# Performance work log

Hardware: AMD Instinct MI355X
Metric: run time of the kernel (lower is better)

Reference implementation:

```python
import jax, jax.numpy as jnp
import numpy as np

BETA = 0.1       # reputation weight
GAMMA = 0.1      # load penalty weight
EXPL_C = 0.1     # UCB exploration constant
LOAD_EMA = 0.9   # load EMA alpha
TOP_K = 2
EPS = 1e-10


def setup_inputs() -> dict:
    key = jax.random.key(0)
    k1, k2, k3, k4, k5 = jax.random.split(key, 5)
    B, S, H, E = 4, 4096, 2048, 64
    return {
        "x": jax.random.normal(k1, (B, S, H), dtype=jnp.float32),
        "gate_w": jax.random.normal(k2, (E, H), dtype=jnp.float32) * (1.0 / np.sqrt(H)),
        "reputation": jax.random.normal(k3, (E,), dtype=jnp.float32),
        "loads": jax.random.uniform(k4, (E,), dtype=jnp.float32),
        "counts": jax.random.uniform(k5, (E,), dtype=jnp.float32),
        "total_decisions": 1000000,
    }


def reference(x, gate_w, reputation, loads, counts, total_decisions):
    B, S, H = x.shape
    E = gate_w.shape[0]
    x_flat = x.reshape(-1, H)                                  # [T, H]
    base_logits = jnp.einsum("th,eh->te", x_flat, gate_w)      # [T, E]

    # current_batch_assignments is None -> current_loads = expert_loads
    updated_loads = LOAD_EMA * loads + (1.0 - LOAD_EMA) * loads  # [E]

    # UCB-style exploration bonus, broadcast over tokens
    expl = EXPL_C * jnp.sqrt(jnp.log(jnp.float32(total_decisions) + 1.0) / (counts + EPS))  # [E]

    selection_scores = (base_logits
                        + BETA * reputation[None, :]
                        - GAMMA * updated_loads[None, :]
                        + expl[None, :])                        # [T, E]

    top_k_scores, top_k_indices = jax.lax.top_k(selection_scores, TOP_K)  # [T, K]
    routing_weights = jax.nn.softmax(top_k_scores, axis=-1).reshape(B, S, TOP_K)
    expert_indices = top_k_indices.reshape(B, S, TOP_K)

    # differentiable load-balancing aux loss
    router_probs = jax.nn.softmax(selection_scores.astype(jnp.float32), axis=-1)  # [T, E]
    expert_gate = jax.nn.one_hot(top_k_indices, E, dtype=jnp.float32).sum(axis=1)  # [T, E]
    tokens_per_expert = expert_gate.mean(axis=0)               # [E]
    router_prob_per_expert = router_probs.mean(axis=0)         # [E]
    aux_loss = (tokens_per_expert * router_prob_per_expert).sum() * E

    return routing_weights, expert_indices, aux_loss
```

## Files before the change

kernel.cpp:

```cpp
#include <hip/hip_runtime.h>
#include <hip/hip_bf16.h>
#include <cmath>

#define HDIM 2048
#define H4   (HDIM / 4)
#define NEXP 64
#define TTOT 16384
#define BKC  64
#define NCHUNK (HDIM / BKC)
#define BTOK 32
#define NBLK (TTOT / BTOK)
#define LDT  72
#define LDS_SC 65

typedef unsigned short u16;
typedef short  bf16x8 __attribute__((ext_vector_type(8)));
typedef float  f32x16 __attribute__((ext_vector_type(16)));

#define WS_AUX_FLOATS  (2 * NBLK * NEXP)
#define WS_GWS_OFF     WS_AUX_FLOATS
#define GWS_FLOATS     (3 * NEXP * HDIM / 2)
#define WS_NEEDED_FLOATS (WS_GWS_OFF + GWS_FLOATS)
#define ESTR (NEXP * HDIM)

__device__ __forceinline__ unsigned cvtpk(float a, float b) {
    __hip_bfloat162 h2 = __float22bfloat162_rn(make_float2(a, b));
    unsigned r;
    __builtin_memcpy(&r, &h2, sizeof(r));
    return r;
}
__device__ __forceinline__ void split3(float4 f, uint2* H, uint2* M, uint2* L) {
    unsigned h0 = cvtpk(f.x, f.y), h1 = cvtpk(f.z, f.w);
    float r0 = f.x - __uint_as_float(h0 << 16);
    float r1 = f.y - __uint_as_float(h0 & 0xffff0000u);
    float r2 = f.z - __uint_as_float(h1 << 16);
    float r3 = f.w - __uint_as_float(h1 & 0xffff0000u);
    unsigned m0 = cvtpk(r0, r1), m1 = cvtpk(r2, r3);
    float s0 = r0 - __uint_as_float(m0 << 16);
    float s1 = r1 - __uint_as_float(m0 & 0xffff0000u);
    float s2 = r2 - __uint_as_float(m1 << 16);
    float s3 = r3 - __uint_as_float(m1 & 0xffff0000u);
    unsigned l0 = cvtpk(s0, s1), l1 = cvtpk(s2, s3);
    *H = make_uint2(h0, h1); *M = make_uint2(m0, m1); *L = make_uint2(l0, l1);
}

__global__ __launch_bounds__(256) void split_gw_k(
    const float* __restrict__ gw, u16* __restrict__ gws)
{
    const int i = blockIdx.x * 256 + threadIdx.x;
    float4 f = reinterpret_cast<const float4*>(gw)[i];
    uint2 h, m, l;
    split3(f, &h, &m, &l);
    reinterpret_cast<uint2*>(gws)[i]            = h;
    reinterpret_cast<uint2*>(gws + ESTR)[i]     = m;
    reinterpret_cast<uint2*>(gws + 2 * ESTR)[i] = l;
}

__global__ __launch_bounds__(256, 2) void router_fused2(
    const float* __restrict__ x,
    const u16*   __restrict__ gws,
    const float* __restrict__ rep,
    const float* __restrict__ loads,
    const float* __restrict__ counts,
    const int*   __restrict__ total_dec,
    float* __restrict__ out_w,
    float* __restrict__ out_idx,
    float* __restrict__ prob_part,
    float* __restrict__ gate_part)
{
    __shared__ __align__(16) char pool[(3 * BTOK * LDT + 3 * NEXP * LDT) * sizeof(short)];
    short (*aT)[BTOK][LDT] = reinterpret_cast<short (*)[BTOK][LDT]>(pool);
    short (*bT)[NEXP][LDT] =
        reinterpret_cast<short (*)[NEXP][LDT]>(pool + 3 * BTOK * LDT * sizeof(short));
    float (*sc_s)[LDS_SC] = reinterpret_cast<float (*)[LDS_SC]>(pool);
    __shared__ float bias_s[NEXP];
    __shared__ float m_s[BTOK], zi_s[BTOK];
    __shared__ int   i1_s[BTOK], i2_s[BTOK];

    const int tid  = threadIdx.x;
    const int lane = tid & 63;
    const int l31  = lane & 31;
    const int lhi  = lane >> 5;
    const int w    = tid >> 6;
    const int wn   = w & 1;
    const int kh   = w >> 1;
    const int rt   = blockIdx.x;
    const int T0   = rt * BTOK;

    if (tid < NEXP) {
        float L = logf((float)(*total_dec) + 1.0f);
        bias_s[tid] = 0.1f * rep[tid] - 0.1f * loads[tid]
                    + 0.1f * sqrtf(L / (counts[tid] + 1e-10f));
    }

    const int srow = tid >> 3;
    const int scol = tid & 7;
    const int grow = tid >> 2;
    const int gcol = tid & 3;

    const float4* __restrict__ x4 = reinterpret_cast<const float4*>(x)
        + (size_t)(T0 + srow) * H4 + scol * 2;
    const u16* __restrict__ gwsB = gws + (size_t)grow * HDIM + gcol * 16;

    f32x16 acc;
    #pragma unroll
    for (int i = 0; i < 16; ++i) acc[i] = 0.0f;

    const short* aP[3];
    const short* bP[3];
    #pragma unroll
    for (int v = 0; v < 3; ++v) {
        aP[v] = &aT[v][l31][8 * lhi];
        bP[v] = &bT[v][32 * wn + l31][8 * lhi];
    }

    float4 xa[2][2];

#define LOAD_CHUNK(CH, SLOT) do {                                              \
        xa[SLOT][0] = x4[(CH) * 16];                                           \
        xa[SLOT][1] = x4[(CH) * 16 + 1];                                       \
    } while (0)

    LOAD_CHUNK(0, 0);
    LOAD_CHUNK(1, 1);

    for (int ch = 0; ch < NCHUNK; ++ch) {
        const int slot = ch & 1;
        uint4 bq[3][2];
        #pragma unroll
        for (int v = 0; v < 3; ++v) {
            const u16* p = gwsB + (size_t)v * ESTR + ch * BKC;
            bq[v][0] = *reinterpret_cast<const uint4*>(p);
            bq[v][1] = *reinterpret_cast<const uint4*>(p + 8);
        }
        {
            uint2 h0, m0, l0, h1, m1, l1;
            split3(xa[slot][0], &h0, &m0, &l0);
            split3(xa[slot][1], &h1, &m1, &l1);
            const int kl = scol * 8;
            *reinterpret_cast<uint4*>(&aT[0][srow][kl]) =
                make_uint4(h0.x, h0.y, h1.x, h1.y);
            *reinterpret_cast<uint4*>(&aT[1][srow][kl]) =
                make_uint4(m0.x, m0.y, m1.x, m1.y);
            *reinterpret_cast<uint4*>(&aT[2][srow][kl]) =
                make_uint4(l0.x, l0.y, l1.x, l1.y);
        }
        if (ch + 2 < NCHUNK) LOAD_CHUNK(ch + 2, slot);
        #pragma unroll
        for (int v = 0; v < 3; ++v) {
            *reinterpret_cast<uint4*>(&bT[v][grow][gcol * 16])     = bq[v][0];
            *reinterpret_cast<uint4*>(&bT[v][grow][gcol * 16 + 8]) = bq[v][1];
        }
        __syncthreads();

        #pragma unroll
        for (int s = 0; s < 2; ++s) {
            const int ko = 16 * (2 * kh + s);
            bf16x8 ah = *reinterpret_cast<const bf16x8*>(aP[0] + ko);
            bf16x8 am = *reinterpret_cast<const bf16x8*>(aP[1] + ko);
            bf16x8 al = *reinterpret_cast<const bf16x8*>(aP[2] + ko);
            bf16x8 bh = *reinterpret_cast<const bf16x8*>(bP[0] + ko);
            bf16x8 bm = *reinterpret_cast<const bf16x8*>(bP[1] + ko);
            bf16x8 bl = *reinterpret_cast<const bf16x8*>(bP[2] + ko);
            acc = __builtin_amdgcn_mfma_f32_32x32x16_bf16(ah, bh, acc, 0, 0, 0);
            acc = __builtin_amdgcn_mfma_f32_32x32x16_bf16(ah, bm, acc, 0, 0, 0);
            acc = __builtin_amdgcn_mfma_f32_32x32x16_bf16(am, bh, acc, 0, 0, 0);
            acc = __builtin_amdgcn_mfma_f32_32x32x16_bf16(ah, bl, acc, 0, 0, 0);
            acc = __builtin_amdgcn_mfma_f32_32x32x16_bf16(am, bm, acc, 0, 0, 0);
            acc = __builtin_amdgcn_mfma_f32_32x32x16_bf16(al, bh, acc, 0, 0, 0);
        }
        __syncthreads();
    }
#undef LOAD_CHUNK

    const int e = 32 * wn + l31;
    if (kh == 0) {
        #pragma unroll
        for (int r = 0; r < 16; ++r) {
            const int t_loc = (r & 3) + 8 * (r >> 2) + 4 * lhi;
            sc_s[t_loc][e] = acc[r];
        }
    }
    __syncthreads();
    if (kh == 1) {
        #pragma unroll
        for (int r = 0; r < 16; ++r) {
            const int t_loc = (r & 3) + 8 * (r >> 2) + 4 * lhi;
            sc_s[t_loc][e] += acc[r] + bias_s[e];
        }
    }
    __syncthreads();

    if (tid < BTOK) {
        const int t = tid;
        float m1 = -INFINITY, m2 = -INFINITY;
        int   i1 = 0, i2 = 0;
        for (int ee = 0; ee < NEXP; ++ee) {
            const float s = sc_s[t][ee];
            if (s > m1)      { m2 = m1; i2 = i1; m1 = s; i1 = ee; }
            else if (s > m2) { m2 = s; i2 = ee; }
        }
        float z = 0.0f;
        for (int ee = 0; ee < NEXP; ++ee) z += __expf(sc_s[t][ee] - m1);

        const float e2  = expf(m2 - m1);
        const float inv = 1.0f / (1.0f + e2);
        const int   gt  = T0 + t;
        reinterpret_cast<float2*>(out_w)[gt]   = make_float2(inv, e2 * inv);
        reinterpret_cast<float2*>(out_idx)[gt] = make_float2((float)i1, (float)i2);
        m_s[t] = m1; zi_s[t] = 1.0f / z; i1_s[t] = i1; i2_s[t] = i2;
    }
    __syncthreads();

    if (tid < NEXP) {
        const int ee = tid;
        float ps = 0.0f, gs = 0.0f;
        for (int t = 0; t < BTOK; ++t) {
            ps += __expf(sc_s[t][ee] - m_s[t]) * zi_s[t];
            gs += (float)((i1_s[t] == ee) + (i2_s[t] == ee));
        }
        prob_part[rt * NEXP + ee] = ps;
        gate_part[rt * NEXP + ee] = gs;
    }
}

__global__ __launch_bounds__(256) void router_aux2(
    const float* __restrict__ prob_part,
    const float* __restrict__ gate_part,
    float* __restrict__ out_aux)
{
    __shared__ float rp[4][NEXP], rg[4][NEXP];
    const int e = threadIdx.x & 63;
    const int q = threadIdx.x >> 6;
    float sp = 0.0f, sg = 0.0f;
    for (int b = q * (NBLK / 4); b < (q + 1) * (NBLK / 4); ++b) {
        sp += prob_part[b * NEXP + e];
        sg += gate_part[b * NEXP + e];
    }
    rp[q][e] = sp; rg[q][e] = sg;
    __syncthreads();
    if (threadIdx.x < NEXP) {
        float pT = rp[0][e] + rp[1][e] + rp[2][e] + rp[3][e];
        float gT = rg[0][e] + rg[1][e] + rg[2][e] + rg[3][e];
        const float invT = 1.0f / (float)TTOT;
        float v = (gT * invT) * (pT * invT);
        #pragma unroll
        for (int off = 32; off > 0; off >>= 1)
            v += __shfl_down(v, off);
        if (e == 0) out_aux[0] = v * (float)NEXP;
    }
}

#define BKF  32
#define LDAF (64 + 4)
__global__ __launch_bounds__(256) void router_main(
    const float* __restrict__ x,
    const float* __restrict__ gw,
    const float* __restrict__ rep,
    const float* __restrict__ loads,
    const float* __restrict__ counts,
    const int*   __restrict__ total_dec,
    float* __restrict__ out_w,
    float* __restrict__ out_idx,
    float* __restrict__ prob_acc,
    float* __restrict__ gate_acc)
{
    __shared__ float a_s[2][BKF][LDAF];
    __shared__ float b_s[2][BKF][LDAF];
    __shared__ float sc_s[64][LDS_SC];
    __shared__ float bias_s[NEXP];
    __shared__ float m_s[64], z_s[64];
    __shared__ int   i1_s[64], i2_s[64];

    const int tid = threadIdx.x;
    const int tx  = tid & 15;
    const int ty  = tid >> 4;
    const int r0  = tid >> 3;
    const int c4  = tid & 7;
    const int t0  = blockIdx.x * 64;

    if (tid < NEXP) {
        float L = logf((float)(*total_dec) + 1.0f);
        bias_s[tid] = 0.1f * rep[tid] - 0.1f * loads[tid]
                    + 0.1f * sqrtf(L / (counts[tid] + 1e-10f));
    }

    const float4* __restrict__ x4 = reinterpret_cast<const float4*>(x) + (size_t)t0 * H4;
    const float4* __restrict__ g4 = reinterpret_cast<const float4*>(gw);

    float acc[4][4] = {};

#define STORE_TILE(BUFI, A0, A1, B0, B1) do {                                  \
        float _t0[4] = {(A0).x, (A0).y, (A0).z, (A0).w};                       \
        float _t1[4] = {(A1).x, (A1).y, (A1).z, (A1).w};                       \
        float _t2[4] = {(B0).x, (B0).y, (B0).z, (B0).w};                       \
        float _t3[4] = {(B1).x, (B1).y, (B1).z, (B1).w};                       \
        _Pragma("unroll")                                                      \
        for (int u = 0; u < 4; ++u) {                                          \
            a_s[BUFI][c4 * 4 + u][r0]      = _t0[u];                           \
            a_s[BUFI][c4 * 4 + u][r0 + 32] = _t1[u];                           \
            b_s[BUFI][c4 * 4 + u][r0]      = _t2[u];                           \
            b_s[BUFI][c4 * 4 + u][r0 + 32] = _t3[u];                           \
        } } while (0)

    {
        float4 a0 = x4[(size_t)r0 * H4 + c4];
        float4 a1 = x4[(size_t)(r0 + 32) * H4 + c4];
        float4 b0 = g4[(size_t)r0 * H4 + c4];
        float4 b1 = g4[(size_t)(r0 + 32) * H4 + c4];
        STORE_TILE(0, a0, a1, b0, b1);
    }
    __syncthreads();

    int buf = 0;
    for (int it = 0; it < HDIM / BKF; ++it) {
        float4 na0, na1, nb0, nb1;
        const bool has_next = (it + 1 < HDIM / BKF);
        if (has_next) {
            const int k4 = (it + 1) * (BKF / 4);
            na0 = x4[(size_t)r0 * H4 + k4 + c4];
            na1 = x4[(size_t)(r0 + 32) * H4 + k4 + c4];
            nb0 = g4[(size_t)r0 * H4 + k4 + c4];
            nb1 = g4[(size_t)(r0 + 32) * H4 + k4 + c4];
        }
        #pragma unroll
        for (int kk = 0; kk < BKF; ++kk) {
            const float4 afv = *reinterpret_cast<const float4*>(&a_s[buf][kk][ty * 4]);
            const float4 bfv = *reinterpret_cast<const float4*>(&b_s[buf][kk][tx * 4]);
            const float af[4] = {afv.x, afv.y, afv.z, afv.w};
            const float bf[4] = {bfv.x, bfv.y, bfv.z, bfv.w};
            #pragma unroll
            for (int i = 0; i < 4; ++i)
                #pragma unroll
                for (int j = 0; j < 4; ++j)
                    acc[i][j] = fmaf(af[i], bf[j], acc[i][j]);
        }
        if (has_next) STORE_TILE(buf ^ 1, na0, na1, nb0, nb1);
        __syncthreads();
        buf ^= 1;
    }
#undef STORE_TILE

    #pragma unroll
    for (int i = 0; i < 4; ++i)
        #pragma unroll
        for (int j = 0; j < 4; ++j)
            sc_s[ty * 4 + i][tx * 4 + j] = acc[i][j] + bias_s[tx * 4 + j];
    __syncthreads();

    if (tid < 64) {
        const int t = tid;
        float m1 = -INFINITY, m2 = -INFINITY;
        int   i1 = 0, i2 = 0;
        for (int e = 0; e < NEXP; ++e) {
            const float s = sc_s[t][e];
            if (s > m1)      { m2 = m1; i2 = i1; m1 = s; i1 = e; }
            else if (s > m2) { m2 = s; i2 = e; }
        }
        float z = 0.0f;
        for (int e = 0; e < NEXP; ++e) z += expf(sc_s[t][e] - m1);
        const float e2  = expf(m2 - m1);
        const float inv = 1.0f / (1.0f + e2);
        const int   gt  = t0 + t;
        reinterpret_cast<float2*>(out_w)[gt]   = make_float2(inv, e2 * inv);
        reinterpret_cast<float2*>(out_idx)[gt] = make_float2((float)i1, (float)i2);
        m_s[t] = m1; z_s[t] = z; i1_s[t] = i1; i2_s[t] = i2;
    }
    __syncthreads();

    if (tid < NEXP) {
        const int e = tid;
        float ps = 0.0f, gs = 0.0f;
        for (int t = 0; t < 64; ++t) {
            ps += expf(sc_s[t][e] - m_s[t]) / z_s[t];
            gs += (float)((i1_s[t] == e) + (i2_s[t] == e));
        }
        atomicAdd(&prob_acc[e], ps);
        atomicAdd(&gate_acc[e], gs);
    }
}

__global__ void router_aux(const float* __restrict__ prob_acc,
                           const float* __restrict__ gate_acc,
                           float* __restrict__ out_aux)
{
    const float invT = 1.0f / (float)TTOT;
    const int e = threadIdx.x;
    float v = (gate_acc[e] * invT) * (prob_acc[e] * invT);
    #pragma unroll
    for (int off = 32; off > 0; off >>= 1)
        v += __shfl_down(v, off);
    if (e == 0) out_aux[0] = v * (float)NEXP;
}

extern "C" void kernel_launch(void* const* d_in, const int* in_sizes, int n_in,
                              void* d_out, int out_size, void* d_ws, size_t ws_size,
                              hipStream_t stream)
{
    const float* x      = (const float*)d_in[0];
    const float* gw     = (const float*)d_in[1];
    const float* rep    = (const float*)d_in[2];
    const float* loads  = (const float*)d_in[3];
    const float* counts = (const float*)d_in[4];
    const int*   total  = (const int*)d_in[5];

    float* out     = (float*)d_out;
    float* out_w   = out;
    float* out_idx = out + 32768;
    float* out_aux = out + 65536;

    if (ws_size >= (size_t)WS_NEEDED_FLOATS * sizeof(float)) {
        float* prob_part = (float*)d_ws;
        float* gate_part = prob_part + NBLK * NEXP;
        u16*   gws       = (u16*)((float*)d_ws + WS_GWS_OFF);

        split_gw_k<<<dim3(NEXP * HDIM / 4 / 256), dim3(256), 0, stream>>>(gw, gws);
        router_fused2<<<dim3(NBLK), dim3(256), 0, stream>>>(
            x, gws, rep, loads, counts, total, out_w, out_idx, prob_part, gate_part);
        router_aux2<<<dim3(1), dim3(256), 0, stream>>>(prob_part, gate_part, out_aux);
    } else {
        float* prob_acc = (float*)d_ws;
        float* gate_acc = prob_acc + NEXP;
        (void)hipMemsetAsync(d_ws, 0, 2 * NEXP * sizeof(float), stream);
        router_main<<<dim3(TTOT / 64), dim3(256), 0, stream>>>(
            x, gw, rep, loads, counts, total, out_w, out_idx, prob_acc, gate_acc);
        router_aux<<<dim3(1), dim3(64), 0, stream>>>(prob_acc, gate_acc, out_aux);
    }
}
```

Before: 251.9 us.

## Double K-chunk size to 128 and prefetch next chunk's x and weights into registers

The K tile per iteration grows from 64 to 128 columns, which halves the number of barrier-separated iterations and doubles the MFMA work between syncs. The prefetch scheme also changes. Instead of a two-deep x register pipeline with weights loaded at the top of each iteration, both x and split weights for the next chunk are now issued right after the barrier and overlap the MFMAs. The cost is more registers (4 float4 plus 12 uint4 held live) and more LDS (about 52KB per block), which may endanger the 2-blocks-per-CU occupancy target.

```diff
diff --git a/kernel.cpp b/kernel.cpp
--- a/kernel.cpp
+++ b/kernel.cpp
@@ -6,11 +6,11 @@
 #define H4   (HDIM / 4)
 #define NEXP 64
 #define TTOT 16384
-#define BKC  64
+#define BKC  128
 #define NCHUNK (HDIM / BKC)
 #define BTOK 32
 #define NBLK (TTOT / BTOK)
-#define LDT  72
+#define LDT  136
 #define LDS_SC 65
 
 typedef unsigned short u16;
@@ -56,7 +56,7 @@
     reinterpret_cast<uint2*>(gws + 2 * ESTR)[i] = l;
 }
 
-__global__ __launch_bounds__(256, 2) void router_fused2(
+__global__ __launch_bounds__(256, 2) void router_fused3(
     const float* __restrict__ x,
     const u16*   __restrict__ gws,
     const float* __restrict__ rep,
@@ -99,8 +99,8 @@
     const int gcol = tid & 3;
 
     const float4* __restrict__ x4 = reinterpret_cast<const float4*>(x)
-        + (size_t)(T0 + srow) * H4 + scol * 2;
-    const u16* __restrict__ gwsB = gws + (size_t)grow * HDIM + gcol * 16;
+        + (size_t)(T0 + srow) * H4 + scol * 4;
+    const u16* __restrict__ gwsB = gws + (size_t)grow * HDIM + gcol * 32;
 
     f32x16 acc;
     #pragma unroll
@@ -114,30 +114,32 @@
         bP[v] = &bT[v][32 * wn + l31][8 * lhi];
     }
 
-    float4 xa[2][2];
-
-#define LOAD_CHUNK(CH, SLOT) do {                                              \
-        xa[SLOT][0] = x4[(CH) * 16];                                           \
-        xa[SLOT][1] = x4[(CH) * 16 + 1];                                       \
+    float4 xa[4];
+    uint4  bq[3][4];
+
+#define LOAD_X(CH) do {                                                        \
+        _Pragma("unroll")                                                      \
+        for (int j = 0; j < 4; ++j) xa[j] = x4[(CH) * (BKC / 4) + j];          \
     } while (0)
-
-    LOAD_CHUNK(0, 0);
-    LOAD_CHUNK(1, 1);
+#define LOAD_B(CH) do {                                                        \
+        _Pragma("unroll")                                                      \
+        for (int v = 0; v < 3; ++v)                                            \
+            _Pragma("unroll")                                                  \
+            for (int j = 0; j < 4; ++j)                                        \
+                bq[v][j] = *reinterpret_cast<const uint4*>(                    \
+                    gwsB + (size_t)v * ESTR + (CH) * BKC + j * 8);             \
+    } while (0)
+
+    LOAD_X(0);
+    LOAD_B(0);
 
     for (int ch = 0; ch < NCHUNK; ++ch) {
-        const int slot = ch & 1;
-        uint4 bq[3][2];
-        #pragma unroll
-        for (int v = 0; v < 3; ++v) {
-            const u16* p = gwsB + (size_t)v * ESTR + ch * BKC;
-            bq[v][0] = *reinterpret_cast<const uint4*>(p);
-            bq[v][1] = *reinterpret_cast<const uint4*>(p + 8);
-        }
-        {
+        #pragma unroll
+        for (int jp = 0; jp < 2; ++jp) {
             uint2 h0, m0, l0, h1, m1, l1;
-            split3(xa[slot][0], &h0, &m0, &l0);
-            split3(xa[slot][1], &h1, &m1, &l1);
-            const int kl = scol * 8;
+            split3(xa[2 * jp],     &h0, &m0, &l0);
+            split3(xa[2 * jp + 1], &h1, &m1, &l1);
+            const int kl = scol * 16 + jp * 8;
             *reinterpret_cast<uint4*>(&aT[0][srow][kl]) =
                 make_uint4(h0.x, h0.y, h1.x, h1.y);
             *reinterpret_cast<uint4*>(&aT[1][srow][kl]) =
@@ -145,17 +147,18 @@
             *reinterpret_cast<uint4*>(&aT[2][srow][kl]) =
                 make_uint4(l0.x, l0.y, l1.x, l1.y);
         }
-        if (ch + 2 < NCHUNK) LOAD_CHUNK(ch + 2, slot);
-        #pragma unroll
-        for (int v = 0; v < 3; ++v) {
-            *reinterpret_cast<uint4*>(&bT[v][grow][gcol * 16])     = bq[v][0];
-            *reinterpret_cast<uint4*>(&bT[v][grow][gcol * 16 + 8]) = bq[v][1];
-        }
+        #pragma unroll
+        for (int v = 0; v < 3; ++v)
+            #pragma unroll
+            for (int j = 0; j < 4; ++j)
+                *reinterpret_cast<uint4*>(&bT[v][grow][gcol * 32 + j * 8]) = bq[v][j];
         __syncthreads();
 
-        #pragma unroll
-        for (int s = 0; s < 2; ++s) {
-            const int ko = 16 * (2 * kh + s);
+        if (ch + 1 < NCHUNK) { LOAD_X(ch + 1); LOAD_B(ch + 1); }
+
+        #pragma unroll
+        for (int s = 0; s < 4; ++s) {
+            const int ko = 16 * (4 * kh + s);
             bf16x8 ah = *reinterpret_cast<const bf16x8*>(aP[0] + ko);
             bf16x8 am = *reinterpret_cast<const bf16x8*>(aP[1] + ko);
             bf16x8 al = *reinterpret_cast<const bf16x8*>(aP[2] + ko);
@@ -171,7 +174,8 @@
         }
         __syncthreads();
     }
-#undef LOAD_CHUNK
+#undef LOAD_X
+#undef LOAD_B
 
     const int e = 32 * wn + l31;
     if (kh == 0) {
@@ -415,7 +419,7 @@
         u16*   gws       = (u16*)((float*)d_ws + WS_GWS_OFF);
 
         split_gw_k<<<dim3(NEXP * HDIM / 4 / 256), dim3(256), 0, stream>>>(gw, gws);
-        router_fused2<<<dim3(NBLK), dim3(256), 0, stream>>>(
+        router_fused3<<<dim3(NBLK), dim3(256), 0, stream>>>(
             x, gws, rep, loads, counts, total, out_w, out_idx, prob_part, gate_part);
         router_aux2<<<dim3(1), dim3(256), 0, stream>>>(prob_part, gate_part, out_aux);
     } else {
```

Result: slower. 319.5 us (+26.8%).
